# Performance work log

Hardware: AMD Instinct MI355X
Metric: run time of the kernel (lower is better)

Reference implementation:

```python
import jax, jax.numpy as jnp
import numpy as np

TOKENS, IN_F, OUT_F = 8192, 4096, 4096
ZERO_POINT = 0      # input zero point (int8)
OUT_ZP = 0          # output zero point (int8)
OUT_SCALE = 0.05    # output quant scale


def setup_inputs() -> dict:
    key = jax.random.key(0)
    k1, k2, k3, k4 = jax.random.split(key, 4)
    x = jax.random.randint(k1, (TOKENS, IN_F), -128, 128, dtype=jnp.int32).astype(jnp.int8)
    # weight stored as [in_features, out_features] (module.weight.t() quantized in from_float)
    weight = jax.random.randint(k2, (IN_F, OUT_F), -127, 128, dtype=jnp.int32).astype(jnp.int8)
    bias = jax.random.randint(k3, (1, OUT_F), -1000, 1000, dtype=jnp.int32)
    gemm_scales = jax.random.uniform(k4, (1, OUT_F), minval=1e-4, maxval=2e-4, dtype=jnp.float32)
    return {"x": x, "weight": weight, "bias": bias, "gemm_scales": gemm_scales}


def reference(x, weight, bias, gemm_scales):
    # int8 -> int32 -> fp32, subtract input zero point
    a = (x.astype(jnp.int32) - ZERO_POINT).astype(jnp.float32)   # [T, IN]
    w = weight.astype(jnp.float32)                               # [IN, OUT]
    gemm_o = (a @ w + bias.astype(jnp.float32)) * gemm_scales / OUT_SCALE  # [T, OUT]
    out = jnp.clip(gemm_o + OUT_ZP, -128, 127).astype(jnp.int8)
    return out
```

## Files before the change

### kernel.cpp

```cpp
#include <hip/hip_runtime.h>
#include <stdint.h>

#define TOKENS 8192
#define IN_F   4096
#define OUT_F  4096

#define BM 256
#define BN 256
#define BK 64
#define NK (IN_F / BK)
#define THREADS 1024

typedef int v4i __attribute__((ext_vector_type(4)));

#define GLOBAL_AS __attribute__((address_space(1)))
#define LDS_AS    __attribute__((address_space(3)))

__global__ __launch_bounds__(256) void pack_x_kernel(const int* __restrict__ x32,
                                                     uint8_t* __restrict__ x8) {
  int t = blockIdx.x * 256 + threadIdx.x;
  const int4 v = ((const int4*)x32)[t];
  uint32_t p = (uint32_t)(v.x & 0xFF)
             | ((uint32_t)(v.y & 0xFF) << 8)
             | ((uint32_t)(v.z & 0xFF) << 16)
             | ((uint32_t)(v.w & 0xFF) << 24);
  ((uint32_t*)x8)[t] = p;
}

__global__ __launch_bounds__(256) void packT_w_kernel(const int* __restrict__ w32,
                                                      uint8_t* __restrict__ wt8) {
  int tn = (blockIdx.x & 63) * 64;
  int tk = (blockIdx.x >> 6) * 64;
  int t = threadIdx.x;
  int n  = tn + (t >> 2);
  int k0 = tk + (t & 3) * 16;
  uint32_t words[4];
#pragma unroll
  for (int w = 0; w < 4; ++w) {
    uint32_t acc = 0;
#pragma unroll
    for (int j = 0; j < 4; ++j) {
      int val = w32[(size_t)(k0 + w * 4 + j) * OUT_F + n];
      acc |= (uint32_t)(val & 0xFF) << (8 * j);
    }
    words[w] = acc;
  }
  uint4 o = make_uint4(words[0], words[1], words[2], words[3]);
  *(uint4*)(wt8 + (size_t)n * IN_F + k0) = o;
}

__global__ __launch_bounds__(THREADS, 4) void gemm_i8_kernel(const uint8_t* __restrict__ A,
                                                             const uint8_t* __restrict__ BT,
                                                             const int* __restrict__ bias,
                                                             const float* __restrict__ scales,
                                                             int* __restrict__ out) {
  __shared__ __align__(16) uint8_t lds[4 * 32768];

  const int t    = threadIdx.x;
  const int lane = t & 63;
  const int w    = t >> 6;
  const int wm   = w >> 2;
  const int wn   = w & 3;
  const int fr   = lane & 15;
  const int fq   = lane >> 4;

  int bid = blockIdx.x;
  int swz = (bid & 7) * 64 + (bid >> 3);
  int bm = swz >> 4;
  int bn = swz & 15;

  const int half = t >> 9;
  const int tt   = t & 511;
  const int lsz  = tt ^ ((tt >> 3) & 7);
  const int srow = half * 128 + (lsz >> 2);
  const int scol = (lsz & 3) * 16;
  const size_t gA = (size_t)(bm * BM + srow) * IN_F + scol;
  const size_t gB = (size_t)(bn * BN + srow) * IN_F + scol;
  const int ldst = half * 8192 + tt * 16;

  auto stage = [&](int j) {
    uint8_t* sb = lds + (j & 3) * 32768;
    const int k0 = j * BK;
    __builtin_amdgcn_global_load_lds((const GLOBAL_AS void*)(A + gA + k0),
                                     (LDS_AS void*)(sb + ldst),          16, 0, 0);
    __builtin_amdgcn_global_load_lds((const GLOBAL_AS void*)(BT + gB + k0),
                                     (LDS_AS void*)(sb + 16384 + ldst),  16, 0, 0);
  };

  int aoff[4], boff[4];
#pragma unroll
  for (int m = 0; m < 4; ++m) {
    int row = wm * 64 + m * 16 + fr;
    int hh = row >> 7, rl = row & 127;
    int b = rl * 64 + fq * 16;
    b ^= ((rl >> 1) & 7) << 4;
    aoff[m] = hh * 8192 + b;
  }
#pragma unroll
  for (int n = 0; n < 4; ++n) {
    int row = wn * 64 + n * 16 + fr;
    int hh = row >> 7, rl = row & 127;
    int b = rl * 64 + fq * 16;
    b ^= ((rl >> 1) & 7) << 4;
    boff[n] = 16384 + hh * 8192 + b;
  }

  v4i acc[4][4];
  const v4i vzero = {0, 0, 0, 0};
#pragma unroll
  for (int m = 0; m < 4; ++m)
#pragma unroll
    for (int n = 0; n < 4; ++n) acc[m][n] = vzero;

  stage(0); stage(1); stage(2);

#define ITER(i, VM, DOSTAGE)                                                    \
  {                                                                             \
    asm volatile("s_waitcnt vmcnt(" #VM ")" ::: "memory");                      \
    asm volatile("s_barrier" ::: "memory");                                     \
    if (DOSTAGE) stage((i) + 3);                                                \
    const uint8_t* sb = lds + ((i) & 3) * 32768;                                \
    v4i af[4], bf[4];                                                           \
    _Pragma("unroll") for (int m = 0; m < 4; ++m)                               \
      af[m] = *(const v4i*)(sb + aoff[m]);                                      \
    _Pragma("unroll") for (int n = 0; n < 4; ++n)                               \
      bf[n] = *(const v4i*)(sb + boff[n]);                                      \
    __builtin_amdgcn_s_setprio(1);                                              \
    _Pragma("unroll") for (int m = 0; m < 4; ++m)                               \
      _Pragma("unroll") for (int n = 0; n < 4; ++n)                             \
        acc[m][n] = __builtin_amdgcn_mfma_i32_16x16x64_i8(af[m], bf[n],         \
                                                          acc[m][n], 0, 0, 0);  \
    __builtin_amdgcn_s_setprio(0);                                              \
  }

  for (int i = 0; i < NK - 3; ++i) {
    ITER(i, 4, true)
  }
  ITER(NK - 3, 4, false)
  ITER(NK - 2, 2, false)
  ITER(NK - 1, 0, false)
#undef ITER

#pragma unroll
  for (int n = 0; n < 4; ++n) {
    const int gn  = bn * BN + wn * 64 + n * 16 + fr;
    const int bsv = bias[gn];
    const float sc = scales[gn] * 20.0f;
#pragma unroll
    for (int m = 0; m < 4; ++m) {
      const int gm0 = bm * BM + wm * 64 + m * 16 + fq * 4;
#pragma unroll
      for (int r = 0; r < 4; ++r) {
        float g = (float)(acc[m][n][r] + bsv) * sc;
        g = fminf(fmaxf(g, -128.0f), 127.0f);
        out[(size_t)(gm0 + r) * OUT_F + gn] = (int)g;
      }
    }
  }
}

extern "C" void kernel_launch(void* const* d_in, const int* in_sizes, int n_in,
                              void* d_out, int out_size, void* d_ws, size_t ws_size,
                              hipStream_t stream) {
  const int*   x32    = (const int*)d_in[0];
  const int*   w32    = (const int*)d_in[1];
  const int*   bias   = (const int*)d_in[2];
  const float* scales = (const float*)d_in[3];
  int* out = (int*)d_out;

  uint8_t* x8  = (uint8_t*)d_ws;
  uint8_t* wt8 = (uint8_t*)d_ws + (size_t)TOKENS * IN_F;

  pack_x_kernel<<<(TOKENS * IN_F / 4) / 256, 256, 0, stream>>>(x32, x8);
  packT_w_kernel<<<(OUT_F / 64) * (IN_F / 64), 256, 0, stream>>>(w32, wt8);
  gemm_i8_kernel<<<(TOKENS / BM) * (OUT_F / BN), THREADS, 0, stream>>>(x8, wt8, bias, scales, out);
}
```

Baseline: 187.5 us.

## Load B fragments directly from global into registers and merge pack kernels

The GEMM now stages only the A tile through LDS. Each wave loads its B fragments straight from global memory into registers, double-buffered one k-step ahead. This halves LDS traffic and footprint per stage, which could raise occupancy, but B reads are no longer shared across the wm waves, so global/L2 traffic for B grows. The two pack kernels are also fused into one launch to save a launch.

```diff
diff --git a/kernel.cpp b/kernel.cpp
--- a/kernel.cpp
+++ b/kernel.cpp
@@ -10,43 +10,47 @@
 #define BK 64
 #define NK (IN_F / BK)
 #define THREADS 1024
+#define SLOT 16384
 
 typedef int v4i __attribute__((ext_vector_type(4)));
 
 #define GLOBAL_AS __attribute__((address_space(1)))
 #define LDS_AS    __attribute__((address_space(3)))
 
-__global__ __launch_bounds__(256) void pack_x_kernel(const int* __restrict__ x32,
-                                                     uint8_t* __restrict__ x8) {
-  int t = blockIdx.x * 256 + threadIdx.x;
-  const int4 v = ((const int4*)x32)[t];
-  uint32_t p = (uint32_t)(v.x & 0xFF)
-             | ((uint32_t)(v.y & 0xFF) << 8)
-             | ((uint32_t)(v.z & 0xFF) << 16)
-             | ((uint32_t)(v.w & 0xFF) << 24);
-  ((uint32_t*)x8)[t] = p;
-}
-
-__global__ __launch_bounds__(256) void packT_w_kernel(const int* __restrict__ w32,
-                                                      uint8_t* __restrict__ wt8) {
-  int tn = (blockIdx.x & 63) * 64;
-  int tk = (blockIdx.x >> 6) * 64;
-  int t = threadIdx.x;
-  int n  = tn + (t >> 2);
-  int k0 = tk + (t & 3) * 16;
-  uint32_t words[4];
+#define XBLOCKS (TOKENS * IN_F / 4 / 256)
+__global__ __launch_bounds__(256) void pack_kernel(const int* __restrict__ x32,
+                                                   uint8_t* __restrict__ x8,
+                                                   const int* __restrict__ w32,
+                                                   uint8_t* __restrict__ wt8) {
+  if (blockIdx.x < XBLOCKS) {
+    int t = blockIdx.x * 256 + threadIdx.x;
+    const int4 v = ((const int4*)x32)[t];
+    uint32_t p = (uint32_t)(v.x & 0xFF)
+               | ((uint32_t)(v.y & 0xFF) << 8)
+               | ((uint32_t)(v.z & 0xFF) << 16)
+               | ((uint32_t)(v.w & 0xFF) << 24);
+    ((uint32_t*)x8)[t] = p;
+  } else {
+    int b = blockIdx.x - XBLOCKS;
+    int tn = (b & 63) * 64;
+    int tk = (b >> 6) * 64;
+    int t = threadIdx.x;
+    int n  = tn + (t >> 2);
+    int k0 = tk + (t & 3) * 16;
+    uint32_t words[4];
 #pragma unroll
-  for (int w = 0; w < 4; ++w) {
-    uint32_t acc = 0;
+    for (int w = 0; w < 4; ++w) {
+      uint32_t acc = 0;
 #pragma unroll
-    for (int j = 0; j < 4; ++j) {
-      int val = w32[(size_t)(k0 + w * 4 + j) * OUT_F + n];
-      acc |= (uint32_t)(val & 0xFF) << (8 * j);
+      for (int j = 0; j < 4; ++j) {
+        int val = w32[(size_t)(k0 + w * 4 + j) * OUT_F + n];
+        acc |= (uint32_t)(val & 0xFF) << (8 * j);
+      }
+      words[w] = acc;
     }
-    words[w] = acc;
+    uint4 o = make_uint4(words[0], words[1], words[2], words[3]);
+    *(uint4*)(wt8 + (size_t)n * IN_F + k0) = o;
   }
-  uint4 o = make_uint4(words[0], words[1], words[2], words[3]);
-  *(uint4*)(wt8 + (size_t)n * IN_F + k0) = o;
 }
 
 __global__ __launch_bounds__(THREADS, 4) void gemm_i8_kernel(const uint8_t* __restrict__ A,
@@ -54,7 +58,7 @@
                                                              const int* __restrict__ bias,
                                                              const float* __restrict__ scales,
                                                              int* __restrict__ out) {
-  __shared__ __align__(16) uint8_t lds[4 * 32768];
+  __shared__ __align__(16) uint8_t lds[4 * SLOT];
 
   const int t    = threadIdx.x;
   const int lane = t & 63;
@@ -75,35 +79,24 @@
   const int srow = half * 128 + (lsz >> 2);
   const int scol = (lsz & 3) * 16;
   const size_t gA = (size_t)(bm * BM + srow) * IN_F + scol;
-  const size_t gB = (size_t)(bn * BN + srow) * IN_F + scol;
   const int ldst = half * 8192 + tt * 16;
 
-  auto stage = [&](int j) {
-    uint8_t* sb = lds + (j & 3) * 32768;
-    const int k0 = j * BK;
-    __builtin_amdgcn_global_load_lds((const GLOBAL_AS void*)(A + gA + k0),
-                                     (LDS_AS void*)(sb + ldst),          16, 0, 0);
-    __builtin_amdgcn_global_load_lds((const GLOBAL_AS void*)(BT + gB + k0),
-                                     (LDS_AS void*)(sb + 16384 + ldst),  16, 0, 0);
+  auto stageA = [&](int j) {
+    __builtin_amdgcn_global_load_lds((const GLOBAL_AS void*)(A + gA + j * BK),
+                                     (LDS_AS void*)(lds + (j & 3) * SLOT + ldst),
+                                     16, 0, 0);
   };
 
-  int aoff[4], boff[4];
-#pragma unroll
-  for (int m = 0; m < 4; ++m) {
-    int row = wm * 64 + m * 16 + fr;
-    int hh = row >> 7, rl = row & 127;
-    int b = rl * 64 + fq * 16;
-    b ^= ((rl >> 1) & 7) << 4;
-    aoff[m] = hh * 8192 + b;
-  }
-#pragma unroll
-  for (int n = 0; n < 4; ++n) {
-    int row = wn * 64 + n * 16 + fr;
-    int hh = row >> 7, rl = row & 127;
-    int b = rl * 64 + fq * 16;
-    b ^= ((rl >> 1) & 7) << 4;
-    boff[n] = 16384 + hh * 8192 + b;
-  }
+  const int row0 = wm * 64 + fr;
+  const int hh = row0 >> 7, rl = row0 & 127;
+  int ab = hh * 8192 + rl * 64 + fq * 16;
+  ab ^= ((rl >> 1) & 7) << 4;
+
+  const uint8_t* gB = BT + (size_t)(bn * BN + wn * 64 + fr) * IN_F + fq * 16;
+
+#define LOADB(j, dst)                                                           \
+  _Pragma("unroll") for (int n = 0; n < 4; ++n)                                 \
+    dst[n] = *(const v4i*)(gB + (size_t)n * (16 * IN_F) + (size_t)(j) * BK);
 
   v4i acc[4][4];
   const v4i vzero = {0, 0, 0, 0};
@@ -112,34 +105,45 @@
 #pragma unroll
     for (int n = 0; n < 4; ++n) acc[m][n] = vzero;
 
-  stage(0); stage(1); stage(2);
+  v4i bC[4], bN_[4];
 
-#define ITER(i, VM, DOSTAGE)                                                    \
+  LOADB(0, bC)
+  stageA(0); stageA(1); stageA(2);
+  asm volatile("s_waitcnt vmcnt(2)" ::: "memory");
+  asm volatile("s_barrier" ::: "memory");
+
+#define BODY(i, DOSTAGE, DOB, bCUR, bNXT)                                       \
   {                                                                             \
-    asm volatile("s_waitcnt vmcnt(" #VM ")" ::: "memory");                      \
-    asm volatile("s_barrier" ::: "memory");                                     \
-    if (DOSTAGE) stage((i) + 3);                                                \
-    const uint8_t* sb = lds + ((i) & 3) * 32768;                                \
-    v4i af[4], bf[4];                                                           \
+    if (DOB) { LOADB((i) + 1, bNXT) }                                           \
+    if (DOSTAGE) stageA((i) + 3);                                               \
+    const uint8_t* sb = lds + ((i) & 3) * SLOT;                                 \
+    v4i af[4];                                                                  \
     _Pragma("unroll") for (int m = 0; m < 4; ++m)                               \
-      af[m] = *(const v4i*)(sb + aoff[m]);                                      \
-    _Pragma("unroll") for (int n = 0; n < 4; ++n)                               \
-      bf[n] = *(const v4i*)(sb + boff[n]);                                      \
+      af[m] = *(const v4i*)(sb + ab + m * 1024);                                \
     __builtin_amdgcn_s_setprio(1);                                              \
     _Pragma("unroll") for (int m = 0; m < 4; ++m)                               \
       _Pragma("unroll") for (int n = 0; n < 4; ++n)                             \
-        acc[m][n] = __builtin_amdgcn_mfma_i32_16x16x64_i8(af[m], bf[n],         \
+        acc[m][n] = __builtin_amdgcn_mfma_i32_16x16x64_i8(af[m], bCUR[n],       \
                                                           acc[m][n], 0, 0, 0);  \
     __builtin_amdgcn_s_setprio(0);                                              \
   }
 
-  for (int i = 0; i < NK - 3; ++i) {
-    ITER(i, 4, true)
+#define TAIL(VM)                                                                \
+  asm volatile("s_waitcnt vmcnt(" #VM ")" ::: "memory");                        \
+  asm volatile("s_barrier" ::: "memory");
+
+  BODY(0, true, true, bC, bN_) TAIL(6)
+  for (int i = 1; i < 60; i += 2) {
+    BODY(i,     true, true, bN_, bC) TAIL(5)
+    BODY(i + 1, true, true, bC, bN_) TAIL(5)
   }
-  ITER(NK - 3, 4, false)
-  ITER(NK - 2, 2, false)
-  ITER(NK - 1, 0, false)
-#undef ITER
+  BODY(61, false, true, bN_, bC) TAIL(4)
+  BODY(62, false, true, bC, bN_)
+  asm volatile("s_barrier" ::: "memory");
+  BODY(63, false, false, bN_, bC)
+#undef BODY
+#undef TAIL
+#undef LOADB
 
 #pragma unroll
   for (int n = 0; n < 4; ++n) {
@@ -171,7 +175,6 @@
   uint8_t* x8  = (uint8_t*)d_ws;
   uint8_t* wt8 = (uint8_t*)d_ws + (size_t)TOKENS * IN_F;
 
-  pack_x_kernel<<<(TOKENS * IN_F / 4) / 256, 256, 0, stream>>>(x32, x8);
-  packT_w_kernel<<<(OUT_F / 64) * (IN_F / 64), 256, 0, stream>>>(w32, wt8);
+  pack_kernel<<<XBLOCKS + (OUT_F / 64) * (IN_F / 64), 256, 0, stream>>>(x32, x8, w32, wt8);
   gemm_i8_kernel<<<(TOKENS / BM) * (OUT_F / BN), THREADS, 0, stream>>>(x8, wt8, bias, scales, out);
 }
```

Result: slower. 348.6 us (+85.9%).

## Replace per-iteration barriers with LDS flag spin-sync and merge pack kernels

Applied to the files above, without the earlier changes.

Merges the two input packing kernels into a single launch that dispatches on block index, removing one kernel launch. In the GEMM main loop, the per-iteration s_barrier is replaced by LDS atomic counters. Each wave signals when its own global-to-LDS loads land and when it has finished reading a buffer, then spins on those counters before computing or overwriting a stage. This lets waves drift apart instead of locking together each K step. The cost is busy-wait spinning on LDS atomics and more fragile memory ordering, since global_load_lds completion and visibility across waves must be handled correctly.

```diff
diff --git a/kernel.cpp b/kernel.cpp
--- a/kernel.cpp
+++ b/kernel.cpp
@@ -16,37 +16,40 @@
 #define GLOBAL_AS __attribute__((address_space(1)))
 #define LDS_AS    __attribute__((address_space(3)))
 
-__global__ __launch_bounds__(256) void pack_x_kernel(const int* __restrict__ x32,
-                                                     uint8_t* __restrict__ x8) {
-  int t = blockIdx.x * 256 + threadIdx.x;
-  const int4 v = ((const int4*)x32)[t];
-  uint32_t p = (uint32_t)(v.x & 0xFF)
-             | ((uint32_t)(v.y & 0xFF) << 8)
-             | ((uint32_t)(v.z & 0xFF) << 16)
-             | ((uint32_t)(v.w & 0xFF) << 24);
-  ((uint32_t*)x8)[t] = p;
-}
-
-__global__ __launch_bounds__(256) void packT_w_kernel(const int* __restrict__ w32,
-                                                      uint8_t* __restrict__ wt8) {
-  int tn = (blockIdx.x & 63) * 64;
-  int tk = (blockIdx.x >> 6) * 64;
-  int t = threadIdx.x;
-  int n  = tn + (t >> 2);
-  int k0 = tk + (t & 3) * 16;
-  uint32_t words[4];
-#pragma unroll
-  for (int w = 0; w < 4; ++w) {
-    uint32_t acc = 0;
-#pragma unroll
-    for (int j = 0; j < 4; ++j) {
-      int val = w32[(size_t)(k0 + w * 4 + j) * OUT_F + n];
-      acc |= (uint32_t)(val & 0xFF) << (8 * j);
+#define XBLOCKS (TOKENS * IN_F / 4 / 256)
+__global__ __launch_bounds__(256) void pack_kernel(const int* __restrict__ x32,
+                                                   uint8_t* __restrict__ x8,
+                                                   const int* __restrict__ w32,
+                                                   uint8_t* __restrict__ wt8) {
+  if (blockIdx.x < XBLOCKS) {
+    int t = blockIdx.x * 256 + threadIdx.x;
+    const int4 v = ((const int4*)x32)[t];
+    uint32_t p = (uint32_t)(v.x & 0xFF)
+               | ((uint32_t)(v.y & 0xFF) << 8)
+               | ((uint32_t)(v.z & 0xFF) << 16)
+               | ((uint32_t)(v.w & 0xFF) << 24);
+    ((uint32_t*)x8)[t] = p;
+  } else {
+    int b = blockIdx.x - XBLOCKS;
+    int tn = (b & 63) * 64;
+    int tk = (b >> 6) * 64;
+    int t = threadIdx.x;
+    int n  = tn + (t >> 2);
+    int k0 = tk + (t & 3) * 16;
+    uint32_t words[4];
+#pragma unroll
+    for (int w = 0; w < 4; ++w) {
+      uint32_t acc = 0;
+#pragma unroll
+      for (int j = 0; j < 4; ++j) {
+        int val = w32[(size_t)(k0 + w * 4 + j) * OUT_F + n];
+        acc |= (uint32_t)(val & 0xFF) << (8 * j);
+      }
+      words[w] = acc;
     }
-    words[w] = acc;
-  }
-  uint4 o = make_uint4(words[0], words[1], words[2], words[3]);
-  *(uint4*)(wt8 + (size_t)n * IN_F + k0) = o;
+    uint4 o = make_uint4(words[0], words[1], words[2], words[3]);
+    *(uint4*)(wt8 + (size_t)n * IN_F + k0) = o;
+  }
 }
 
 __global__ __launch_bounds__(THREADS, 4) void gemm_i8_kernel(const uint8_t* __restrict__ A,
@@ -55,6 +58,7 @@
                                                              const float* __restrict__ scales,
                                                              int* __restrict__ out) {
   __shared__ __align__(16) uint8_t lds[4 * 32768];
+  __shared__ int flg[8];
 
   const int t    = threadIdx.x;
   const int lane = t & 63;
@@ -112,14 +116,53 @@
 #pragma unroll
     for (int n = 0; n < 4; ++n) acc[m][n] = vzero;
 
+#define SIGNAL(idx)                                                             \
+  if (lane == 0) __hip_atomic_fetch_add(&flg[idx], 1, __ATOMIC_RELEASE,         \
+                                        __HIP_MEMORY_SCOPE_WORKGROUP);
+#define SPIN(idx, tgt)                                                          \
+  while (__hip_atomic_load(&flg[idx], __ATOMIC_ACQUIRE,                         \
+                           __HIP_MEMORY_SCOPE_WORKGROUP) < (tgt)) { }           \
+  asm volatile("" ::: "memory");
+
+  if (t < 8) flg[t] = 0;
+  __syncthreads();
+
   stage(0); stage(1); stage(2);
-
-#define ITER(i, VM, DOSTAGE)                                                    \
+  asm volatile("s_waitcnt vmcnt(4)" ::: "memory");
+  SIGNAL(0)
+
+  for (int j = 0; j <= 60; ++j) {
+    asm volatile("s_waitcnt vmcnt(2)" ::: "memory");
+    SIGNAL((j + 1) & 3)
+    SPIN(j & 3, ((j >> 2) + 1) * 16)
+    const uint8_t* sb = lds + (j & 3) * 32768;
+    v4i af[4], bf[4];
+#pragma unroll
+    for (int m = 0; m < 4; ++m) af[m] = *(const v4i*)(sb + aoff[m]);
+#pragma unroll
+    for (int n = 0; n < 4; ++n) bf[n] = *(const v4i*)(sb + boff[n]);
+    __builtin_amdgcn_s_setprio(1);
+#pragma unroll
+    for (int m = 0; m < 4; ++m)
+#pragma unroll
+      for (int n = 0; n < 4; ++n)
+        acc[m][n] = __builtin_amdgcn_mfma_i32_16x16x64_i8(af[m], bf[n],
+                                                          acc[m][n], 0, 0, 0);
+    __builtin_amdgcn_s_setprio(0);
+    asm volatile("s_waitcnt lgkmcnt(0)" ::: "memory");
+    SIGNAL(4 + (j & 3))
+    SPIN(4 + ((j + 3) & 3), ((j + 3) >> 2) * 16)
+    stage(j + 3);
+  }
+
+#define TAILIT(j, VM, DOSIG)                                                    \
   {                                                                             \
-    asm volatile("s_waitcnt vmcnt(" #VM ")" ::: "memory");                      \
-    asm volatile("s_barrier" ::: "memory");                                     \
-    if (DOSTAGE) stage((i) + 3);                                                \
-    const uint8_t* sb = lds + ((i) & 3) * 32768;                                \
+    if (DOSIG) {                                                                \
+      asm volatile("s_waitcnt vmcnt(" #VM ")" ::: "memory");                    \
+      SIGNAL(((j) + 1) & 3)                                                     \
+    }                                                                           \
+    SPIN((j) & 3, (((j) >> 2) + 1) * 16)                                        \
+    const uint8_t* sb = lds + ((j) & 3) * 32768;                                \
     v4i af[4], bf[4];                                                           \
     _Pragma("unroll") for (int m = 0; m < 4; ++m)                               \
       af[m] = *(const v4i*)(sb + aoff[m]);                                      \
@@ -133,13 +176,12 @@
     __builtin_amdgcn_s_setprio(0);                                              \
   }
 
-  for (int i = 0; i < NK - 3; ++i) {
-    ITER(i, 4, true)
-  }
-  ITER(NK - 3, 4, false)
-  ITER(NK - 2, 2, false)
-  ITER(NK - 1, 0, false)
-#undef ITER
+  TAILIT(61, 2, true)
+  TAILIT(62, 0, true)
+  TAILIT(63, 0, false)
+#undef TAILIT
+#undef SIGNAL
+#undef SPIN
 
 #pragma unroll
   for (int n = 0; n < 4; ++n) {
@@ -171,7 +213,6 @@
   uint8_t* x8  = (uint8_t*)d_ws;
   uint8_t* wt8 = (uint8_t*)d_ws + (size_t)TOKENS * IN_F;
 
-  pack_x_kernel<<<(TOKENS * IN_F / 4) / 256, 256, 0, stream>>>(x32, x8);
-  packT_w_kernel<<<(OUT_F / 64) * (IN_F / 64), 256, 0, stream>>>(w32, wt8);
+  pack_kernel<<<XBLOCKS + (OUT_F / 64) * (IN_F / 64), 256, 0, stream>>>(x32, x8, w32, wt8);
   gemm_i8_kernel<<<(TOKENS / BM) * (OUT_F / BN), THREADS, 0, stream>>>(x8, wt8, bias, scales, out);
 }
```

After: 240.6 us. 28.3% more time.

## Switch int8 GEMM to 32x32x32 MFMA tiles and merge pack kernels

Applied to the files above, without the earlier changes.

Replaces the 4x4 grid of 16x16x64 int8 MFMAs per wave with a 2x2 grid of 32x32x32 MFMAs split over two k-substeps, reworking the LDS fragment offsets, accumulator layout and epilogue row mapping to match. The larger MFMA shape halves the number of LDS fragment loads per wave for the same output tile and may reach higher matrix throughput. It also fuses the two input packing kernels into one launch to save a kernel launch. The new epilogue writes rows in a strided 4+8 pattern, and the accumulator layout has to match the 32x32 MFMA output layout for results to be correct.

```diff
diff --git a/kernel.cpp b/kernel.cpp
--- a/kernel.cpp
+++ b/kernel.cpp
@@ -11,42 +11,46 @@
 #define NK (IN_F / BK)
 #define THREADS 1024
 
-typedef int v4i __attribute__((ext_vector_type(4)));
+typedef int v4i  __attribute__((ext_vector_type(4)));
+typedef int v16i __attribute__((ext_vector_type(16)));
 
 #define GLOBAL_AS __attribute__((address_space(1)))
 #define LDS_AS    __attribute__((address_space(3)))
 
-__global__ __launch_bounds__(256) void pack_x_kernel(const int* __restrict__ x32,
-                                                     uint8_t* __restrict__ x8) {
-  int t = blockIdx.x * 256 + threadIdx.x;
-  const int4 v = ((const int4*)x32)[t];
-  uint32_t p = (uint32_t)(v.x & 0xFF)
-             | ((uint32_t)(v.y & 0xFF) << 8)
-             | ((uint32_t)(v.z & 0xFF) << 16)
-             | ((uint32_t)(v.w & 0xFF) << 24);
-  ((uint32_t*)x8)[t] = p;
-}
-
-__global__ __launch_bounds__(256) void packT_w_kernel(const int* __restrict__ w32,
-                                                      uint8_t* __restrict__ wt8) {
-  int tn = (blockIdx.x & 63) * 64;
-  int tk = (blockIdx.x >> 6) * 64;
-  int t = threadIdx.x;
-  int n  = tn + (t >> 2);
-  int k0 = tk + (t & 3) * 16;
-  uint32_t words[4];
+#define XBLOCKS (TOKENS * IN_F / 4 / 256)
+__global__ __launch_bounds__(256) void pack_kernel(const int* __restrict__ x32,
+                                                   uint8_t* __restrict__ x8,
+                                                   const int* __restrict__ w32,
+                                                   uint8_t* __restrict__ wt8) {
+  if (blockIdx.x < XBLOCKS) {
+    int t = blockIdx.x * 256 + threadIdx.x;
+    const int4 v = ((const int4*)x32)[t];
+    uint32_t p = (uint32_t)(v.x & 0xFF)
+               | ((uint32_t)(v.y & 0xFF) << 8)
+               | ((uint32_t)(v.z & 0xFF) << 16)
+               | ((uint32_t)(v.w & 0xFF) << 24);
+    ((uint32_t*)x8)[t] = p;
+  } else {
+    int b = blockIdx.x - XBLOCKS;
+    int tn = (b & 63) * 64;
+    int tk = (b >> 6) * 64;
+    int t = threadIdx.x;
+    int n  = tn + (t >> 2);
+    int k0 = tk + (t & 3) * 16;
+    uint32_t words[4];
 #pragma unroll
-  for (int w = 0; w < 4; ++w) {
-    uint32_t acc = 0;
+    for (int w = 0; w < 4; ++w) {
+      uint32_t acc = 0;
 #pragma unroll
-    for (int j = 0; j < 4; ++j) {
-      int val = w32[(size_t)(k0 + w * 4 + j) * OUT_F + n];
-      acc |= (uint32_t)(val & 0xFF) << (8 * j);
+      for (int j = 0; j < 4; ++j) {
+        int val = w32[(size_t)(k0 + w * 4 + j) * OUT_F + n];
+        acc |= (uint32_t)(val & 0xFF) << (8 * j);
+      }
+      words[w] = acc;
     }
-    words[w] = acc;
+    uint4 o = make_uint4(words[0], words[1], words[2], words[3]);
+    *(uint4*)(wt8 + (size_t)n * IN_F + k0) = o;
   }
-  uint4 o = make_uint4(words[0], words[1], words[2], words[3]);
-  *(uint4*)(wt8 + (size_t)n * IN_F + k0) = o;
 }
 
 __global__ __launch_bounds__(THREADS, 4) void gemm_i8_kernel(const uint8_t* __restrict__ A,
@@ -61,8 +65,8 @@
   const int w    = t >> 6;
   const int wm   = w >> 2;
   const int wn   = w & 3;
-  const int fr   = lane & 15;
-  const int fq   = lane >> 4;
+  const int fr   = lane & 31;
+  const int hi   = lane >> 5;
 
   int bid = blockIdx.x;
   int swz = (bid & 7) * 64 + (bid >> 3);
@@ -87,30 +91,33 @@
                                      (LDS_AS void*)(sb + 16384 + ldst),  16, 0, 0);
   };
 
-  int aoff[4], boff[4];
+  int aoff[2][2], boff[2][2];
 #pragma unroll
-  for (int m = 0; m < 4; ++m) {
-    int row = wm * 64 + m * 16 + fr;
+  for (int mt = 0; mt < 2; ++mt) {
+    int row = wm * 64 + mt * 32 + fr;
     int hh = row >> 7, rl = row & 127;
-    int b = rl * 64 + fq * 16;
-    b ^= ((rl >> 1) & 7) << 4;
-    aoff[m] = hh * 8192 + b;
+    int sig = ((rl >> 1) & 7) << 4;
+#pragma unroll
+    for (int ks = 0; ks < 2; ++ks)
+      aoff[mt][ks] = hh * 8192 + ((rl * 64 + ks * 32 + hi * 16) ^ sig);
   }
 #pragma unroll
-  for (int n = 0; n < 4; ++n) {
-    int row = wn * 64 + n * 16 + fr;
+  for (int nt = 0; nt < 2; ++nt) {
+    int row = wn * 64 + nt * 32 + fr;
     int hh = row >> 7, rl = row & 127;
-    int b = rl * 64 + fq * 16;
-    b ^= ((rl >> 1) & 7) << 4;
-    boff[n] = 16384 + hh * 8192 + b;
+    int sig = ((rl >> 1) & 7) << 4;
+#pragma unroll
+    for (int ks = 0; ks < 2; ++ks)
+      boff[nt][ks] = 16384 + hh * 8192 + ((rl * 64 + ks * 32 + hi * 16) ^ sig);
   }
 
-  v4i acc[4][4];
-  const v4i vzero = {0, 0, 0, 0};
+  v16i acc[2][2];
 #pragma unroll
-  for (int m = 0; m < 4; ++m)
+  for (int mt = 0; mt < 2; ++mt)
 #pragma unroll
-    for (int n = 0; n < 4; ++n) acc[m][n] = vzero;
+    for (int nt = 0; nt < 2; ++nt)
+#pragma unroll
+      for (int r = 0; r < 16; ++r) acc[mt][nt][r] = 0;
 
   stage(0); stage(1); stage(2);
 
@@ -120,16 +127,19 @@
     asm volatile("s_barrier" ::: "memory");                                     \
     if (DOSTAGE) stage((i) + 3);                                                \
     const uint8_t* sb = lds + ((i) & 3) * 32768;                                \
-    v4i af[4], bf[4];                                                           \
-    _Pragma("unroll") for (int m = 0; m < 4; ++m)                               \
-      af[m] = *(const v4i*)(sb + aoff[m]);                                      \
-    _Pragma("unroll") for (int n = 0; n < 4; ++n)                               \
-      bf[n] = *(const v4i*)(sb + boff[n]);                                      \
+    v4i af[2][2], bf[2][2];                                                     \
+    _Pragma("unroll") for (int mt = 0; mt < 2; ++mt)                            \
+      _Pragma("unroll") for (int ks = 0; ks < 2; ++ks)                          \
+        af[mt][ks] = *(const v4i*)(sb + aoff[mt][ks]);                          \
+    _Pragma("unroll") for (int nt = 0; nt < 2; ++nt)                            \
+      _Pragma("unroll") for (int ks = 0; ks < 2; ++ks)                          \
+        bf[nt][ks] = *(const v4i*)(sb + boff[nt][ks]);                          \
     __builtin_amdgcn_s_setprio(1);                                              \
-    _Pragma("unroll") for (int m = 0; m < 4; ++m)                               \
-      _Pragma("unroll") for (int n = 0; n < 4; ++n)                             \
-        acc[m][n] = __builtin_amdgcn_mfma_i32_16x16x64_i8(af[m], bf[n],         \
-                                                          acc[m][n], 0, 0, 0);  \
+    _Pragma("unroll") for (int ks = 0; ks < 2; ++ks)                            \
+      _Pragma("unroll") for (int mt = 0; mt < 2; ++mt)                          \
+        _Pragma("unroll") for (int nt = 0; nt < 2; ++nt)                        \
+          acc[mt][nt] = __builtin_amdgcn_mfma_i32_32x32x32_i8(                  \
+              af[mt][ks], bf[nt][ks], acc[mt][nt], 0, 0, 0);                    \
     __builtin_amdgcn_s_setprio(0);                                              \
   }
 
@@ -142,18 +152,19 @@
 #undef ITER
 
 #pragma unroll
-  for (int n = 0; n < 4; ++n) {
-    const int gn  = bn * BN + wn * 64 + n * 16 + fr;
+  for (int nt = 0; nt < 2; ++nt) {
+    const int gn  = bn * BN + wn * 64 + nt * 32 + fr;
     const int bsv = bias[gn];
     const float sc = scales[gn] * 20.0f;
 #pragma unroll
-    for (int m = 0; m < 4; ++m) {
-      const int gm0 = bm * BM + wm * 64 + m * 16 + fq * 4;
+    for (int mt = 0; mt < 2; ++mt) {
+      const int gm0 = bm * BM + wm * 64 + mt * 32 + hi * 4;
 #pragma unroll
-      for (int r = 0; r < 4; ++r) {
-        float g = (float)(acc[m][n][r] + bsv) * sc;
+      for (int r = 0; r < 16; ++r) {
+        const int gm = gm0 + (r & 3) + 8 * (r >> 2);
+        float g = (float)(acc[mt][nt][r] + bsv) * sc;
         g = fminf(fmaxf(g, -128.0f), 127.0f);
-        out[(size_t)(gm0 + r) * OUT_F + gn] = (int)g;
+        out[(size_t)gm * OUT_F + gn] = (int)g;
       }
     }
   }
@@ -171,7 +182,6 @@
   uint8_t* x8  = (uint8_t*)d_ws;
   uint8_t* wt8 = (uint8_t*)d_ws + (size_t)TOKENS * IN_F;
 
-  pack_x_kernel<<<(TOKENS * IN_F / 4) / 256, 256, 0, stream>>>(x32, x8);
-  packT_w_kernel<<<(OUT_F / 64) * (IN_F / 64), 256, 0, stream>>>(w32, wt8);
+  pack_kernel<<<XBLOCKS + (OUT_F / 64) * (IN_F / 64), 256, 0, stream>>>(x32, x8, w32, wt8);
   gemm_i8_kernel<<<(TOKENS / BM) * (OUT_F / BN), THREADS, 0, stream>>>(x8, wt8, bias, scales, out);
 }
```

After: 201.1 us. +7.2%, slower.
